# Kernel tuning notes

Measured on AMD Instinct MI355X. Metric: run time of the kernel, lower is better.

Reference implementation:

```python
import jax, jax.numpy as jnp
import numpy as np

# Config (Mamba2-2.7B-like)
HID = 2048          # hidden_size
EXPAND = 2
INTER = EXPAND * HID   # 4096
NH = 64             # num_heads
HD = 64             # head_dim (NH*HD == INTER)
NG = 8              # n_groups
SS = 128            # state_size
CK = 4              # conv_kernel
CH = 256            # chunk_size
EPS = 1e-6
CONV_DIM = INTER + 2 * NG * SS          # 6144
PROJ = INTER + CONV_DIM + NH            # 10304
B_SZ, SEQ = 2, 2048


def segment_sum(x):
    # x: [..., T] -> [..., T, T]; stable cumulative-sum based segment sums
    T = x.shape[-1]
    x = jnp.repeat(x[..., None], T, axis=-1)
    x = jnp.where(jnp.tril(jnp.ones((T, T), dtype=bool), k=-1), x, 0.0)
    s = jnp.cumsum(x, axis=-2)
    return jnp.where(jnp.tril(jnp.ones((T, T), dtype=bool), k=0), s, -jnp.inf)


def setup_inputs() -> dict:
    key = jax.random.key(0)
    ks = jax.random.split(key, 6)
    sc = 0.02
    return {
        "input_states": jax.random.normal(ks[0], (B_SZ, SEQ, HID), dtype=jnp.float32),
        "in_proj_w": jax.random.normal(ks[1], (HID, PROJ), dtype=jnp.float32) * sc,
        "conv_w": jax.random.normal(ks[2], (CK, 1, CONV_DIM), dtype=jnp.float32) * sc,  # WIO, depthwise
        "conv_b": jnp.zeros((CONV_DIM,), dtype=jnp.float32),
        "dt_bias": jnp.ones((NH,), dtype=jnp.float32),
        "A_log": jnp.log(jnp.arange(1, NH + 1, dtype=jnp.float32)),
        "D": jnp.ones((NH,), dtype=jnp.float32),
        "norm_w": jnp.ones((INTER,), dtype=jnp.float32),
        "out_proj_w": jax.random.normal(ks[3], (INTER, HID), dtype=jnp.float32) * sc,
    }


def reference(input_states, in_proj_w, conv_w, conv_b, dt_bias, A_log, D, norm_w, out_proj_w):
    b, s, _ = input_states.shape
    proj = input_states @ in_proj_w                                   # [b,s,PROJ]
    gate, hBC, dt = jnp.split(proj, [INTER, INTER + CONV_DIM], axis=-1)

    # depthwise causal-ish conv (flax nn.Conv with padding='SAME', groups=CONV_DIM)
    hBC = jax.lax.conv_general_dilated(
        hBC, conv_w, window_strides=(1,), padding="SAME",
        dimension_numbers=("NWC", "WIO", "NWC"), feature_group_count=CONV_DIM,
    ) + conv_b
    hBC = jax.nn.silu(hBC)[:, :s]
    hs, Bmat, Cmat = jnp.split(hBC, [INTER, INTER + NG * SS], axis=-1)

    A = -jnp.exp(A_log.astype(jnp.float32))                           # [h]
    dt = jax.nn.softplus(dt + dt_bias)                                # [b,s,h]
    dt = jnp.maximum(dt, 0.0)                                         # time_step_limit (0, inf)

    hs = hs.reshape(b, s, NH, HD).astype(jnp.float32)                 # [b,s,h,p]
    Bmat = Bmat.reshape(b, s, NG, SS).astype(jnp.float32)
    Cmat = Cmat.reshape(b, s, NG, SS).astype(jnp.float32)
    Bmat = jnp.repeat(Bmat, NH // NG, axis=2)                         # [b,s,h,n]
    Cmat = jnp.repeat(Cmat, NH // NG, axis=2)

    pad = (CH - s % CH) % CH

    def to_chunks(t):
        t = jnp.pad(t, [(0, 0), (0, pad)] + [(0, 0)] * (t.ndim - 2))
        return t.reshape(b, -1, CH, *t.shape[2:])

    D_res = D[None, None, :, None] * jnp.pad(hs, [(0, 0), (0, pad), (0, 0), (0, 0)])

    hs_dt = hs * dt[..., None]                                        # discretize x
    A_bt = A[None, None, :] * dt                                      # [b,s,h]

    hs_c = to_chunks(hs_dt)                                           # [b,c,l,h,p]
    A_c = to_chunks(A_bt)                                             # [b,c,l,h]
    B_c = to_chunks(Bmat)                                             # [b,c,l,h,n]
    C_c = to_chunks(Cmat)

    A_p = jnp.transpose(A_c, (0, 3, 1, 2))                            # [b,h,c,l]
    A_cum = jnp.cumsum(A_p, axis=-1)

    # 1. intra-chunk (diagonal blocks)
    L = jnp.exp(segment_sum(A_p))                                     # [b,h,c,l,l]
    M = jnp.einsum("bclhn,bcshn->bclsh", C_c, B_c) * jnp.transpose(L, (0, 2, 3, 4, 1))
    Y_diag = jnp.einsum("bclsh,bcshp->bclhp", M, hs_c)

    # 2. intra-chunk states
    decay_states = jnp.exp(A_cum[..., -1:] - A_cum)                   # [b,h,c,l]
    B_decay = B_c * jnp.transpose(decay_states, (0, 2, 3, 1))[..., None]
    states = jnp.einsum("bclhn,bclhp->bchpn", B_decay, hs_c)          # [b,c,h,p,n]

    # 3. inter-chunk recurrence
    states = jnp.concatenate([jnp.zeros_like(states[:, :1]), states], axis=1)  # [b,c+1,h,p,n]
    A_last = jnp.pad(A_cum[..., -1], [(0, 0), (0, 0), (1, 0)])        # [b,h,c+1]
    decay_chunk = jnp.exp(segment_sum(A_last))                        # [b,h,c+1,c+1]
    new_states = jnp.einsum("bhij,bjhpn->bihpn", decay_chunk, states)
    states_out = new_states[:, :-1]                                   # [b,c,h,p,n]

    # 4. state -> output
    state_decay_out = jnp.exp(A_cum)                                  # [b,h,c,l]
    Y_off = jnp.einsum("bclhn,bchpn->bclhp", C_c, states_out) \
        * jnp.transpose(state_decay_out, (0, 2, 3, 1))[..., None]

    y = (Y_diag + Y_off).reshape(b, -1, NH, HD) + D_res
    y = y[:, :s].reshape(b, s, INTER)

    # gated RMSNorm
    yf = y.astype(jnp.float32) * jax.nn.silu(gate.astype(jnp.float32))
    var = jnp.mean(jnp.square(yf), axis=-1, keepdims=True)
    yn = norm_w * (yf * jax.lax.rsqrt(var + EPS))

    return (yn.astype(input_states.dtype)) @ out_proj_w
```

## Files before the change

kernel.cpp:

```cpp
#include <hip/hip_runtime.h>
#include <hip/hip_bf16.h>


#define S_LEN 2048
#define HIDDEN 2048
#define INTER 4096
#define NH 64
#define HD 64
#define NG 8
#define SSZ 128
#define CONV_DIM 6144
#define PROJ_DIM 10304
#define PROJ_PAD 10496
#define NC 8
#define CHK 256
#define ROWS 4096
#define DT_OFF 10240
#define B_OFF 4096
#define C_OFF 5120

typedef __hip_bfloat16 bf16;
typedef __attribute__((ext_vector_type(8))) short bf16x8;
typedef __attribute__((ext_vector_type(4))) float f32x4;
#define MFMA16(a, b, c) __builtin_amdgcn_mfma_f32_16x16x32_bf16(a, b, c, 0, 0, 0)

union U16x8 { uint4 u; bf16x8 v; };

__device__ __forceinline__ float siluf(float x) { return x / (1.f + __expf(-x)); }
__device__ __forceinline__ float ldf(const float* p) { return *p; }
__device__ __forceinline__ float ldf(const bf16* p) { return __bfloat162float(*p); }
__device__ __forceinline__ unsigned short f2bu(float x) {
  bf16 h = __float2bfloat16(x);
  return __builtin_bit_cast(unsigned short, h);
}
__device__ __forceinline__ float bu2f(unsigned short u) {
  return __uint_as_float(((unsigned)u) << 16);
}
__device__ __forceinline__ unsigned pack2(float lo, float hi) {
  return ((unsigned)f2bu(hi) << 16) | f2bu(lo);
}
__device__ __forceinline__ void gload16(const void* g, void* l) {
  __builtin_amdgcn_global_load_lds((const __attribute__((address_space(1))) unsigned*)g,
                                   (__attribute__((address_space(3))) unsigned*)l, 16, 0, 0);
}

__global__ __launch_bounds__(256) void cvt_bf16_k(const float* __restrict__ x,
                                                  unsigned short* __restrict__ o, int n4) {
  int idx = blockIdx.x * 256 + threadIdx.x;
  int stride = gridDim.x * 256;
  for (int i = idx; i < n4; i += stride) {
    float4 v = reinterpret_cast<const float4*>(x)[i];
    uint2 u = make_uint2(pack2(v.x, v.y), pack2(v.z, v.w));
    reinterpret_cast<uint2*>(o)[i] = u;
  }
}

__global__ __launch_bounds__(256) void add_k(const float* __restrict__ p0,
                                             const float* __restrict__ p1,
                                             float* __restrict__ o, int n4) {
  int idx = blockIdx.x * 256 + threadIdx.x;
  int stride = gridDim.x * 256;
  for (int i = idx; i < n4; i += stride) {
    float4 a = reinterpret_cast<const float4*>(p0)[i];
    float4 b = reinterpret_cast<const float4*>(p1)[i];
    reinterpret_cast<float4*>(o)[i] =
        make_float4(a.x + b.x, a.y + b.y, a.z + b.z, a.w + b.w);
  }
}

__global__ __launch_bounds__(256) void wT_k(const float* __restrict__ W,
                                            unsigned short* __restrict__ Wt,
                                            int K, int N) {
  __shared__ unsigned short t[64][72];
  int n0 = blockIdx.x * 64, k0 = blockIdx.y * 64;
  int tid = threadIdx.x;
  const int fr = tid >> 4;
  const int fc = tid & 15;
#pragma unroll
  for (int i = 0; i < 4; ++i) {
    int kr = fr + i * 16;
    int nc = fc * 4;
    int ng = n0 + nc;
    float4 v = (ng < N) ? *reinterpret_cast<const float4*>(&W[(size_t)(k0 + kr) * N + ng])
                        : make_float4(0.f, 0.f, 0.f, 0.f);
    t[kr][nc] = f2bu(v.x); t[kr][nc + 1] = f2bu(v.y);
    t[kr][nc + 2] = f2bu(v.z); t[kr][nc + 3] = f2bu(v.w);
  }
  __syncthreads();
#pragma unroll
  for (int i = 0; i < 2; ++i) {
    int item = tid + i * 256;
    int nr = item >> 3;
    int kc8 = (item & 7) * 8;
    unsigned short vals[8];
#pragma unroll
    for (int ei = 0; ei < 8; ++ei) {
      int e = ei ^ (tid & 7);
      vals[e] = t[kc8 + e][nr];
    }
    *reinterpret_cast<uint4*>(&Wt[(size_t)(n0 + nr) * K + k0 + kc8]) =
        *reinterpret_cast<const uint4*>(vals);
  }
}

__device__ __forceinline__ int mod9(int x) { return x >= 9 ? x - 9 : x; }

__device__ __forceinline__ void stage_half(const unsigned short* __restrict__ A,
                                           const unsigned short* __restrict__ Bt,
                                           unsigned short* lds9, int hj, int slot,
                                           int m0, int n0, int K, int kbase, int hmax,
                                           int tid, int wid) {
  if (hj >= hmax) return;
  const int t = hj >> 2, i = hj & 3;
  const unsigned short* src = (i < 2) ? A : Bt;
  const int br = ((i < 2) ? m0 : n0) + (i & 1) * 128;
  const int g = (tid & 7) ^ ((tid >> 3) & 7);
#pragma unroll
  for (int r = 0; r < 2; ++r) {
    int row = r * 64 + (tid >> 3);
    gload16(&src[(size_t)(br + row) * K + kbase + t * 64 + g * 8],
            &lds9[slot * 8192 + r * 4096 + wid * 512]);
  }
}

template <typename TC>
__global__ __launch_bounds__(512, 2) void gemm_8ph(const unsigned short* __restrict__ A,
                                                   const unsigned short* __restrict__ Bt,
                                                   TC* __restrict__ C,
                                                   int M, int N, int K, int ksplit) {
  extern __shared__ unsigned short lds9[];
  const int tid = threadIdx.x;
  const int lane = tid & 63, hi = lane >> 4, sl = lane & 15;
  const int wid = tid >> 6;
  const int wm = wid >> 2, wn = wid & 3;
  const int gx = gridDim.x;
  int lin = blockIdx.y * gx + blockIdx.x;
  int cpx = (gx * gridDim.y) >> 3;
  int swz = (lin & 7) * cpx + (lin >> 3);
  const int m0 = (swz / gx) * 256;
  const int n0 = (swz % gx) * 256;
  const int kbase = blockIdx.z * ksplit;
  TC* Cz = C + (size_t)blockIdx.z * M * N;
  const int NT = ksplit >> 6;
  const int HMAX = NT << 2;
  const int rbB = (wn & 1) * 64;

  f32x4 acc[8][4] = {};
  bf16x8 a0[4][2], a1[4][2], bb[4][2];

#pragma unroll
  for (int j = 0; j < 5; ++j)
    stage_half(A, Bt, lds9, j, j, m0, n0, K, kbase, HMAX, tid, wid);

  int j0 = 0;
  for (int t = 0; t < NT; ++t) {
    const int sAw = mod9(j0 + wm);
    const int sBw = mod9(j0 + 2 + (wn >> 1));
    if (4 * t + 4 < HMAX) { asm volatile("s_waitcnt vmcnt(2)" ::: "memory"); }
    else                  { asm volatile("s_waitcnt vmcnt(0)" ::: "memory"); }
    __builtin_amdgcn_sched_barrier(0);
    __builtin_amdgcn_s_barrier();
    __builtin_amdgcn_sched_barrier(0);
#pragma unroll
    for (int mf = 0; mf < 4; ++mf)
#pragma unroll
      for (int kk = 0; kk < 2; ++kk) {
        int ra = mf * 16 + sl;
        a0[mf][kk] = *reinterpret_cast<const bf16x8*>(
            &lds9[sAw * 8192 + ra * 64 + (((kk * 4 + hi) ^ (ra & 7)) * 8)]);
      }
#pragma unroll
    for (int nf = 0; nf < 2; ++nf)
#pragma unroll
      for (int kk = 0; kk < 2; ++kk) {
        int rb = rbB + nf * 16 + sl;
        bb[nf][kk] = *reinterpret_cast<const bf16x8*>(
            &lds9[sBw * 8192 + rb * 64 + (((kk * 4 + hi) ^ (rb & 7)) * 8)]);
      }
    stage_half(A, Bt, lds9, 4 * t + 5, mod9(j0 + 5), m0, n0, K, kbase, HMAX, tid, wid);
    asm volatile("s_waitcnt lgkmcnt(0)" ::: "memory");
    __builtin_amdgcn_sched_barrier(0);
    __builtin_amdgcn_s_setprio(1);
#pragma unroll
    for (int mf = 0; mf < 4; ++mf)
#pragma unroll
      for (int nf = 0; nf < 2; ++nf)
#pragma unroll
        for (int kk = 0; kk < 2; ++kk)
          acc[mf][nf] = MFMA16(a0[mf][kk], bb[nf][kk], acc[mf][nf]);
    __builtin_amdgcn_s_setprio(0);
    __builtin_amdgcn_sched_barrier(0);
#pragma unroll
    for (int nf = 2; nf < 4; ++nf)
#pragma unroll
      for (int kk = 0; kk < 2; ++kk) {
        int rb = rbB + nf * 16 + sl;
        bb[nf][kk] = *reinterpret_cast<const bf16x8*>(
            &lds9[sBw * 8192 + rb * 64 + (((kk * 4 + hi) ^ (rb & 7)) * 8)]);
      }
    stage_half(A, Bt, lds9, 4 * t + 6, mod9(j0 + 6), m0, n0, K, kbase, HMAX, tid, wid);
    asm volatile("s_waitcnt lgkmcnt(0)" ::: "memory");
    __builtin_amdgcn_sched_barrier(0);
    __builtin_amdgcn_s_setprio(1);
#pragma unroll
    for (int mf = 0; mf < 4; ++mf)
#pragma unroll
      for (int nf = 2; nf < 4; ++nf)
#pragma unroll
        for (int kk = 0; kk < 2; ++kk)
          acc[mf][nf] = MFMA16(a0[mf][kk], bb[nf][kk], acc[mf][nf]);
    __builtin_amdgcn_s_setprio(0);
    __builtin_amdgcn_sched_barrier(0);
#pragma unroll
    for (int mf = 0; mf < 4; ++mf)
#pragma unroll
      for (int kk = 0; kk < 2; ++kk) {
        int ra = (mf + 4) * 16 + sl;
        a1[mf][kk] = *reinterpret_cast<const bf16x8*>(
            &lds9[sAw * 8192 + ra * 64 + (((kk * 4 + hi) ^ (ra & 7)) * 8)]);
      }
    stage_half(A, Bt, lds9, 4 * t + 7, mod9(j0 + 7), m0, n0, K, kbase, HMAX, tid, wid);
    asm volatile("s_waitcnt lgkmcnt(0)" ::: "memory");
    __builtin_amdgcn_sched_barrier(0);
    __builtin_amdgcn_s_setprio(1);
#pragma unroll
    for (int mf = 0; mf < 4; ++mf)
#pragma unroll
      for (int nf = 0; nf < 2; ++nf)
#pragma unroll
        for (int kk = 0; kk < 2; ++kk)
          acc[mf + 4][nf] = MFMA16(a1[mf][kk], bb[nf][kk], acc[mf + 4][nf]);
    __builtin_amdgcn_s_setprio(0);
    __builtin_amdgcn_sched_barrier(0);
    stage_half(A, Bt, lds9, 4 * t + 8, mod9(j0 + 8), m0, n0, K, kbase, HMAX, tid, wid);
    __builtin_amdgcn_s_setprio(1);
#pragma unroll
    for (int mf = 0; mf < 4; ++mf)
#pragma unroll
      for (int nf = 2; nf < 4; ++nf)
#pragma unroll
        for (int kk = 0; kk < 2; ++kk)
          acc[mf + 4][nf] = MFMA16(a1[mf][kk], bb[nf][kk], acc[mf + 4][nf]);
    __builtin_amdgcn_s_setprio(0);
    __builtin_amdgcn_sched_barrier(0);
    j0 += 4; if (j0 >= 9) j0 -= 9;
  }
#pragma unroll
  for (int mf = 0; mf < 8; ++mf)
#pragma unroll
    for (int nf = 0; nf < 4; ++nf) {
      int col = n0 + wn * 64 + nf * 16 + sl;
      if (col < N) {
#pragma unroll
        for (int r = 0; r < 4; ++r) {
          int row = m0 + wm * 128 + mf * 16 + hi * 4 + r;
          if constexpr (sizeof(TC) == 2)
            Cz[(size_t)row * N + col] = __float2bfloat16(acc[mf][nf][r]);
          else
            Cz[(size_t)row * N + col] = acc[mf][nf][r];
        }
      }
    }
}

__global__ __launch_bounds__(256) void conv_silu_k(const bf16* __restrict__ proj,
                                                   const float* __restrict__ cw,
                                                   const float* __restrict__ cb,
                                                   bf16* __restrict__ convo) {
  int idx = blockIdx.x * 256 + threadIdx.x;
  int ci = idx % (CONV_DIM / 8);
  int row = idx / (CONV_DIM / 8);
  int c8 = ci * 8;
  int t = row & (S_LEN - 1);
  int b = row >> 11;
  float acc[8];
  {
    float4 b0 = *reinterpret_cast<const float4*>(&cb[c8]);
    float4 b1 = *reinterpret_cast<const float4*>(&cb[c8 + 4]);
    acc[0] = b0.x; acc[1] = b0.y; acc[2] = b0.z; acc[3] = b0.w;
    acc[4] = b1.x; acc[5] = b1.y; acc[6] = b1.z; acc[7] = b1.w;
  }
#pragma unroll
  for (int w = 0; w < 4; w++) {
    int tt = t + w - 1;
    if (tt >= 0 && tt < S_LEN) {
      U16x8 u;
      u.u = *reinterpret_cast<const uint4*>(
          &proj[(size_t)(b * S_LEN + tt) * PROJ_DIM + INTER + c8]);
      float4 w0 = *reinterpret_cast<const float4*>(&cw[w * CONV_DIM + c8]);
      float4 w1 = *reinterpret_cast<const float4*>(&cw[w * CONV_DIM + c8 + 4]);
      acc[0] += w0.x * bu2f((unsigned short)u.v[0]);
      acc[1] += w0.y * bu2f((unsigned short)u.v[1]);
      acc[2] += w0.z * bu2f((unsigned short)u.v[2]);
      acc[3] += w0.w * bu2f((unsigned short)u.v[3]);
      acc[4] += w1.x * bu2f((unsigned short)u.v[4]);
      acc[5] += w1.y * bu2f((unsigned short)u.v[5]);
      acc[6] += w1.z * bu2f((unsigned short)u.v[6]);
      acc[7] += w1.w * bu2f((unsigned short)u.v[7]);
    }
  }
  uint4 o;
  o.x = pack2(siluf(acc[0]), siluf(acc[1]));
  o.y = pack2(siluf(acc[2]), siluf(acc[3]));
  o.z = pack2(siluf(acc[4]), siluf(acc[5]));
  o.w = pack2(siluf(acc[6]), siluf(acc[7]));
  *reinterpret_cast<uint4*>(&convo[(size_t)row * CONV_DIM + c8]) = o;
}

__global__ __launch_bounds__(256) void dt_k(const bf16* __restrict__ proj,
                                            const float* __restrict__ dtb,
                                            float* __restrict__ dtp) {
  int idx = blockIdx.x * 256 + threadIdx.x;
  int h = idx & 63;
  int row = idx >> 6;
  float x = ldf(&proj[(size_t)row * PROJ_DIM + DT_OFF + h]) + dtb[h];
  dtp[idx] = (x > 20.f) ? x : log1pf(__expf(x));
}

__global__ __launch_bounds__(256) void acum_k(const float* __restrict__ dtp,
                                              const float* __restrict__ alog,
                                              float* __restrict__ acum) {
  __shared__ float buf[2][CHK];
  int blk = blockIdx.x;
  int c = blk & 7;
  int h = (blk >> 3) & 63;
  int b = blk >> 9;
  int tid = threadIdx.x;
  int row0 = b * S_LEN + c * CHK;
  float a = -__expf(alog[h]);
  buf[0][tid] = a * dtp[(size_t)(row0 + tid) * NH + h];
  __syncthreads();
  int cur = 0;
#pragma unroll
  for (int off = 1; off < 256; off <<= 1) {
    float nv = buf[cur][tid];
    if (tid >= off) nv += buf[cur][tid - off];
    buf[cur ^ 1][tid] = nv;
    cur ^= 1;
    __syncthreads();
  }
  acum[(size_t)blk * CHK + tid] = buf[cur][tid];
}

__global__ __launch_bounds__(256) void chunk_states_mfma(const bf16* __restrict__ convo,
                                                         const float* __restrict__ dtp,
                                                         const float* __restrict__ acum,
                                                         float* __restrict__ cs) {
  __shared__ float sAc[CHK];
  __shared__ float sDtf[CHK];
  __shared__ float sEx[64];
  __shared__ __align__(16) unsigned short sHT[64 * 64];
  __shared__ __align__(16) unsigned short sBd[128 * 64];
  const int tid = threadIdx.x;
  const int lane = tid & 63, hi = lane >> 4, sl = lane & 15;
  const int wid = tid >> 6, wm = wid >> 1, wn = wid & 1;
  const int blk = blockIdx.x;
  const int h = blk & 63, bc = blk >> 6, c = bc & 7, b = bc >> 3, g = h >> 3;
  const int row0 = b * S_LEN + c * CHK;
  sAc[tid] = acum[((size_t)((b * NH + h) * NC + c)) * CHK + tid];
  sDtf[tid] = dtp[(size_t)(row0 + tid) * NH + h];
  f32x4 acc[2][4] = {};
  for (int ts = 0; ts < 4; ++ts) {
    __syncthreads();
    if (tid < 64) sEx[tid] = __expf(sAc[CHK - 1] - sAc[ts * 64 + tid]);
    __syncthreads();
#pragma unroll
    for (int it = 0; it < 2; ++it) {
      int cid = tid + it * 256;
      int t = cid >> 3, p8 = (cid & 7) * 8;
      U16x8 u;
      u.u = *reinterpret_cast<const uint4*>(
          &convo[(size_t)(row0 + ts * 64 + t) * CONV_DIM + h * HD + p8]);
      float dtv = sDtf[ts * 64 + t];
#pragma unroll
      for (int e = 0; e < 8; ++e) {
        int p = p8 + e;
        int G = (p & 7) ^ ((p >> 3) & 7);
        sHT[p * 64 + (((t >> 3) ^ G) * 8) + (t & 7)] =
            f2bu(bu2f((unsigned short)u.v[e]) * dtv);
      }
    }
#pragma unroll
    for (int it = 0; it < 4; ++it) {
      int cid = tid + it * 256;
      int t = cid >> 4, n8 = (cid & 15) * 8;
      U16x8 u;
      u.u = *reinterpret_cast<const uint4*>(
          &convo[(size_t)(row0 + ts * 64 + t) * CONV_DIM + B_OFF + g * SSZ + n8]);
      float ex = sEx[t];
#pragma unroll
      for (int e = 0; e < 8; ++e) {
        int n = n8 + e;
        int G = (n & 7) ^ ((n >> 3) & 7);
        sBd[n * 64 + (((t >> 3) ^ G) * 8) + (t & 7)] =
            f2bu(bu2f((unsigned short)u.v[e]) * ex);
      }
    }
    __syncthreads();
#pragma unroll
    for (int kc = 0; kc < 2; ++kc) {
      bf16x8 a[2], bb[4];
#pragma unroll
      for (int m = 0; m < 2; ++m) {
        int p = wm * 32 + m * 16 + sl;
        int G = (p & 7) ^ ((p >> 3) & 7);
        a[m] = *reinterpret_cast<const bf16x8*>(
            &sHT[p * 64 + (((kc * 4 + hi) ^ G) * 8)]);
      }
#pragma unroll
      for (int j = 0; j < 4; ++j) {
        int n = wn * 64 + j * 16 + sl;
        int G = (n & 7) ^ ((n >> 3) & 7);
        bb[j] = *reinterpret_cast<const bf16x8*>(
            &sBd[n * 64 + (((kc * 4 + hi) ^ G) * 8)]);
      }
#pragma unroll
      for (int m = 0; m < 2; ++m)
#pragma unroll
        for (int j = 0; j < 4; ++j) acc[m][j] = MFMA16(a[m], bb[j], acc[m][j]);
    }
  }
  size_t base = (size_t)blk * HD * SSZ;
#pragma unroll
  for (int m = 0; m < 2; ++m)
#pragma unroll
    for (int j = 0; j < 4; ++j)
#pragma unroll
      for (int r = 0; r < 4; ++r) {
        int p = wm * 32 + m * 16 + hi * 4 + r;
        int n = wn * 64 + j * 16 + sl;
        cs[base + (size_t)p * SSZ + n] = acc[m][j][r];
      }
}

__global__ __launch_bounds__(256) void chunk_rec_k(const float* __restrict__ acum,
                                                   float* __restrict__ cs) {
  int idx = blockIdx.x * 256 + threadIdx.x;
  int n = idx & 127;
  int p = (idx >> 7) & 63;
  int h = (idx >> 13) & 63;
  int b = idx >> 19;
  float run = 0.f;
#pragma unroll
  for (int c = 0; c < NC; c++) {
    size_t off = ((size_t)(((b * NC + c) * NH + h) * HD + p)) * SSZ + n;
    float csv = cs[off];
    float al = acum[((size_t)((b * NH + h) * NC + c)) * CHK + (CHK - 1)];
    cs[off] = run;
    run = run * __expf(al) + csv;
  }
}

__global__ __launch_bounds__(256) void chunk_out_mfma(const bf16* __restrict__ convo,
                                                      const float* __restrict__ dtp,
                                                      const float* __restrict__ acum,
                                                      const float* __restrict__ cs,
                                                      const float* __restrict__ Dp,
                                                      bf16* __restrict__ yb) {
  __shared__ float sAc[CHK];
  __shared__ float sDt[CHK];
  __shared__ __align__(16) unsigned short sB[64 * 128];
  __shared__ __align__(16) unsigned short sH[64 * 64];
  __shared__ __align__(16) unsigned short sW[4 * 64 * 64];
  const int tid = threadIdx.x;
  const int lane = tid & 63, hi = lane >> 4, sl = lane & 15;
  const int wid = tid >> 6;
  const int blk = blockIdx.x;
  const int h = blk & 63;
  const int bc = blk >> 6;
  const int c = bc & 7;
  const int b = bc >> 3;
  const int g = h >> 3;
  const int row0 = b * S_LEN + c * CHK;
  unsigned short* sWp = &sW[wid * 4096];

  sAc[tid] = acum[((size_t)((b * NH + h) * NC + c)) * CHK + tid];
  sDt[tid] = dtp[(size_t)(row0 + tid) * NH + h];

  bf16x8 cf[4][4];
#pragma unroll
  for (int m = 0; m < 4; ++m)
#pragma unroll
    for (int kc = 0; kc < 4; ++kc) {
      int l = wid * 64 + m * 16 + sl;
      U16x8 u;
      u.u = *reinterpret_cast<const uint4*>(
          &convo[(size_t)(row0 + l) * CONV_DIM + C_OFF + g * SSZ + kc * 32 + hi * 8]);
      cf[m][kc] = u.v;
    }

  f32x4 acc[4][4] = {};

  for (int st = 0; st < 4; ++st) {
    __syncthreads();
#pragma unroll
    for (int it = 0; it < 4; ++it) {
      int cid = tid + it * 256;
      int s = cid >> 4, gr = cid & 15;
      const uint4* p = reinterpret_cast<const uint4*>(
          &convo[(size_t)(row0 + st * 64 + s) * CONV_DIM + B_OFF + g * SSZ + gr * 8]);
      *reinterpret_cast<uint4*>(&sB[s * 128 + (gr ^ (s & 7)) * 8]) = *p;
    }
#pragma unroll
    for (int it = 0; it < 16; ++it) {
      int cid = tid + it * 256;
      int s = cid >> 6, pp = cid & 63;
      float v = ldf(&convo[(size_t)(row0 + st * 64 + s) * CONV_DIM + h * HD + pp]) *
                sDt[st * 64 + s];
      sH[pp * 64 + (((s >> 3) ^ (pp & 7)) * 8) + (s & 7)] = f2bu(v);
    }
    __syncthreads();
    if (wid >= st) {
#pragma unroll
      for (int sf = 0; sf < 4; ++sf) {
        f32x4 d[4] = {};
#pragma unroll
        for (int kc = 0; kc < 4; ++kc) {
          int srow = sf * 16 + sl;
          bf16x8 bfv = *reinterpret_cast<const bf16x8*>(
              &sB[srow * 128 + (((kc * 4 + hi) ^ (srow & 7)) * 8)]);
#pragma unroll
          for (int m = 0; m < 4; ++m) d[m] = MFMA16(cf[m][kc], bfv, d[m]);
        }
        int s_loc = sf * 16 + sl;
        int s_glob = st * 64 + s_loc;
        float acS = sAc[s_glob];
        bool diag = (st == wid);
#pragma unroll
        for (int m = 0; m < 4; ++m)
#pragma unroll
          for (int r = 0; r < 4; ++r) {
            int l_loc = m * 16 + hi * 4 + r;
            int l_glob = wid * 64 + l_loc;
            float e = __expf(sAc[l_glob] - acS);
            float v = d[m][r] * e;
            if (diag && s_glob > l_glob) v = 0.f;
            sWp[l_loc * 64 + (((s_loc >> 3) ^ (l_loc & 7)) * 8) + (s_loc & 7)] = f2bu(v);
          }
      }
    }
    __syncthreads();
    if (wid >= st) {
#pragma unroll
      for (int kc = 0; kc < 2; ++kc) {
        bf16x8 a[4], bb[4];
#pragma unroll
        for (int m = 0; m < 4; ++m) {
          int l = m * 16 + sl;
          a[m] = *reinterpret_cast<const bf16x8*>(
              &sWp[l * 64 + (((kc * 4 + hi) ^ (l & 7)) * 8)]);
        }
#pragma unroll
        for (int j = 0; j < 4; ++j) {
          int p = j * 16 + sl;
          bb[j] = *reinterpret_cast<const bf16x8*>(
              &sH[p * 64 + (((kc * 4 + hi) ^ (p & 7)) * 8)]);
        }
#pragma unroll
        for (int m = 0; m < 4; ++m)
#pragma unroll
          for (int j = 0; j < 4; ++j) acc[m][j] = MFMA16(a[m], bb[j], acc[m][j]);
      }
    }
  }

  __syncthreads();
  {
    size_t sinbase = ((size_t)(((b * NC + c) * NH + h) * HD)) * SSZ;
#pragma unroll
    for (int it = 0; it < 8; ++it) {
      int cid = tid + it * 256;
      int p = cid >> 5, q = cid & 31;
      float4 v = *reinterpret_cast<const float4*>(&cs[sinbase + (size_t)p * SSZ + q * 4]);
      uint2 val = make_uint2(pack2(v.x, v.y), pack2(v.z, v.w));
      *reinterpret_cast<uint2*>(&sB[p * 128 + ((q >> 1) ^ (p & 7)) * 8 + (q & 1) * 4]) = val;
    }
  }
  __syncthreads();
#pragma unroll
  for (int m = 0; m < 4; ++m) {
    float e = __expf(sAc[wid * 64 + m * 16 + sl]);
#pragma unroll
    for (int kc = 0; kc < 4; ++kc) {
      bf16x8 fv = cf[m][kc];
#pragma unroll
      for (int ei = 0; ei < 8; ++ei) {
        unsigned short us = (unsigned short)fv[ei];
        fv[ei] = (short)f2bu(bu2f(us) * e);
      }
      cf[m][kc] = fv;
    }
  }
#pragma unroll
  for (int kc = 0; kc < 4; ++kc) {
    bf16x8 bb[4];
#pragma unroll
    for (int j = 0; j < 4; ++j) {
      int p = j * 16 + sl;
      bb[j] = *reinterpret_cast<const bf16x8*>(
          &sB[p * 128 + (((kc * 4 + hi) ^ (p & 7)) * 8)]);
    }
#pragma unroll
    for (int m = 0; m < 4; ++m)
#pragma unroll
      for (int j = 0; j < 4; ++j) acc[m][j] = MFMA16(cf[m][kc], bb[j], acc[m][j]);
  }

  float Dh = Dp[h];
#pragma unroll
  for (int m = 0; m < 4; ++m)
#pragma unroll
    for (int j = 0; j < 4; ++j)
#pragma unroll
      for (int r = 0; r < 4; ++r) {
        int l_glob = wid * 64 + m * 16 + hi * 4 + r;
        size_t row = (size_t)(row0 + l_glob);
        int pg = j * 16 + sl;
        float hraw = ldf(&convo[row * CONV_DIM + h * HD + pg]);
        yb[row * INTER + h * HD + pg] = __float2bfloat16(acc[m][j][r] + Dh * hraw);
      }
}

__global__ __launch_bounds__(256) void norm_k(const bf16* __restrict__ proj,
                                              const float* __restrict__ nw,
                                              bf16* __restrict__ yb) {
  int row = blockIdx.x;
  int tid = threadIdx.x;
  float vals[16];
  float ss = 0.f;
#pragma unroll
  for (int half = 0; half < 2; half++) {
    int colb = tid * 8 + half * 2048;
    U16x8 gy, gg;
    gy.u = *reinterpret_cast<const uint4*>(&yb[(size_t)row * INTER + colb]);
    gg.u = *reinterpret_cast<const uint4*>(&proj[(size_t)row * PROJ_DIM + colb]);
#pragma unroll
    for (int e = 0; e < 8; e++) {
      float yf = bu2f((unsigned short)gy.v[e]) * siluf(bu2f((unsigned short)gg.v[e]));
      vals[half * 8 + e] = yf;
      ss += yf * yf;
    }
  }
#pragma unroll
  for (int off = 32; off > 0; off >>= 1) ss += __shfl_down(ss, off);
  __shared__ float red[4];
  if ((tid & 63) == 0) red[tid >> 6] = ss;
  __syncthreads();
  float tot = red[0] + red[1] + red[2] + red[3];
  float scale = rsqrtf(tot * (1.f / INTER) + 1e-6f);
#pragma unroll
  for (int half = 0; half < 2; half++) {
    int colb = tid * 8 + half * 2048;
    float4 w0 = *reinterpret_cast<const float4*>(&nw[colb]);
    float4 w1 = *reinterpret_cast<const float4*>(&nw[colb + 4]);
    float s0 = vals[half * 8 + 0] * scale * w0.x, s1 = vals[half * 8 + 1] * scale * w0.y;
    float s2 = vals[half * 8 + 2] * scale * w0.z, s3 = vals[half * 8 + 3] * scale * w0.w;
    float s4 = vals[half * 8 + 4] * scale * w1.x, s5 = vals[half * 8 + 5] * scale * w1.y;
    float s6 = vals[half * 8 + 6] * scale * w1.z, s7 = vals[half * 8 + 7] * scale * w1.w;
    uint4 o = make_uint4(pack2(s0, s1), pack2(s2, s3), pack2(s4, s5), pack2(s6, s7));
    *reinterpret_cast<uint4*>(&yb[(size_t)row * INTER + colb]) = o;
  }
}

extern "C" void kernel_launch(void* const* d_in, const int* in_sizes, int n_in,
                              void* d_out, int out_size, void* d_ws, size_t ws_size,
                              hipStream_t stream) {
  const float* x     = (const float*)d_in[0];
  const float* wproj = (const float*)d_in[1];
  const float* cw    = (const float*)d_in[2];
  const float* cb    = (const float*)d_in[3];
  const float* dtb   = (const float*)d_in[4];
  const float* alog  = (const float*)d_in[5];
  const float* Dp    = (const float*)d_in[6];
  const float* nw    = (const float*)d_in[7];
  const float* wout  = (const float*)d_in[8];
  float* out = (float*)d_out;
  char* ws = (char*)d_ws;

  bf16*  proj  = (bf16*)(ws);
  bf16*  convo = (bf16*)(ws + 84410368);
  bf16*  yb    = (bf16*)(ws + 134742016);
  float* dtp   = (float*)(ws + 168296448);
  float* acum  = (float*)(ws + 169345024);
  float* cs    = (float*)(ws + 170393600);
  unsigned short* Wt1 = (unsigned short*)(ws + 84410368);
  unsigned short* xb  = (unsigned short*)(ws + 134742016);
  unsigned short* Wt2 = (unsigned short*)(ws + 170393600);
  float* part = (float*)(ws);

  hipFuncSetAttribute(reinterpret_cast<const void*>(&gemm_8ph<bf16>),
                      hipFuncAttributeMaxDynamicSharedMemorySize, 147456);
  hipFuncSetAttribute(reinterpret_cast<const void*>(&gemm_8ph<float>),
                      hipFuncAttributeMaxDynamicSharedMemorySize, 147456);

  cvt_bf16_k<<<dim3(2048), 256, 0, stream>>>(x, xb, ROWS * HIDDEN / 4);
  wT_k<<<dim3(PROJ_PAD / 64, HIDDEN / 64), 256, 0, stream>>>(wproj, Wt1, HIDDEN, PROJ_DIM);
  gemm_8ph<bf16><<<dim3(PROJ_PAD / 256, ROWS / 256, 1), 512, 147456, stream>>>(
      xb, Wt1, proj, ROWS, PROJ_DIM, HIDDEN, HIDDEN);
  conv_silu_k<<<dim3(ROWS * CONV_DIM / 8 / 256), 256, 0, stream>>>(proj, cw, cb, convo);
  dt_k<<<dim3(ROWS * NH / 256), 256, 0, stream>>>(proj, dtb, dtp);
  acum_k<<<dim3(2 * NH * NC), 256, 0, stream>>>(dtp, alog, acum);
  chunk_states_mfma<<<dim3(2 * NC * NH), 256, 0, stream>>>(convo, dtp, acum, cs);
  chunk_rec_k<<<dim3(2 * NH * HD * SSZ / 256), 256, 0, stream>>>(acum, cs);
  chunk_out_mfma<<<dim3(2 * NC * NH), 256, 0, stream>>>(convo, dtp, acum, cs, Dp, yb);
  norm_k<<<dim3(ROWS), 256, 0, stream>>>(proj, nw, yb);
  wT_k<<<dim3(HIDDEN / 64, INTER / 64), 256, 0, stream>>>(wout, Wt2, INTER, HIDDEN);
  gemm_8ph<float><<<dim3(HIDDEN / 256, ROWS / 256, 2), 512, 147456, stream>>>(
      (const unsigned short*)yb, Wt2, part, ROWS, HIDDEN, INTER, INTER / 2);
  add_k<<<dim3(2048), 256, 0, stream>>>(part, part + (size_t)ROWS * HIDDEN, out,
                                        ROWS * HIDDEN / 4);
}
```

Before: 507.2 us.

## Balance causal chunk_out work across waves with paired 32-row strips

```diff
diff --git a/kernel.cpp b/kernel.cpp
--- a/kernel.cpp
+++ b/kernel.cpp
@@ -459,9 +459,9 @@
                                                       bf16* __restrict__ yb) {
   __shared__ float sAc[CHK];
   __shared__ float sDt[CHK];
-  __shared__ __align__(16) unsigned short sB[64 * 128];
-  __shared__ __align__(16) unsigned short sH[64 * 64];
-  __shared__ __align__(16) unsigned short sW[4 * 64 * 64];
+  __shared__ __align__(16) unsigned short sB[32 * 128];
+  __shared__ __align__(16) unsigned short sH[64 * 32];
+  __shared__ __align__(16) unsigned short sW[8 * 32 * 32];
   const int tid = threadIdx.x;
   const int lane = tid & 63, hi = lane >> 4, sl = lane & 15;
   const int wid = tid >> 6;
@@ -472,95 +472,114 @@
   const int b = bc >> 3;
   const int g = h >> 3;
   const int row0 = b * S_LEN + c * CHK;
-  unsigned short* sWp = &sW[wid * 4096];
+  const int strips[2] = {wid, 7 - wid};
 
   sAc[tid] = acum[((size_t)((b * NH + h) * NC + c)) * CHK + tid];
   sDt[tid] = dtp[(size_t)(row0 + tid) * NH + h];
 
-  bf16x8 cf[4][4];
-#pragma unroll
-  for (int m = 0; m < 4; ++m)
-#pragma unroll
-    for (int kc = 0; kc < 4; ++kc) {
-      int l = wid * 64 + m * 16 + sl;
-      U16x8 u;
-      u.u = *reinterpret_cast<const uint4*>(
-          &convo[(size_t)(row0 + l) * CONV_DIM + C_OFF + g * SSZ + kc * 32 + hi * 8]);
-      cf[m][kc] = u.v;
-    }
-
-  f32x4 acc[4][4] = {};
-
-  for (int st = 0; st < 4; ++st) {
+  bf16x8 cf[2][2][4];
+#pragma unroll
+  for (int t2 = 0; t2 < 2; ++t2)
+#pragma unroll
+    for (int lf = 0; lf < 2; ++lf)
+#pragma unroll
+      for (int kc = 0; kc < 4; ++kc) {
+        int l = strips[t2] * 32 + lf * 16 + sl;
+        U16x8 u;
+        u.u = *reinterpret_cast<const uint4*>(
+            &convo[(size_t)(row0 + l) * CONV_DIM + C_OFF + g * SSZ + kc * 32 + hi * 8]);
+        cf[t2][lf][kc] = u.v;
+      }
+
+  f32x4 acc[2][2][4] = {};
+
+  for (int st = 0; st < 8; ++st) {
     __syncthreads();
 #pragma unroll
-    for (int it = 0; it < 4; ++it) {
+    for (int it = 0; it < 2; ++it) {
       int cid = tid + it * 256;
       int s = cid >> 4, gr = cid & 15;
       const uint4* p = reinterpret_cast<const uint4*>(
-          &convo[(size_t)(row0 + st * 64 + s) * CONV_DIM + B_OFF + g * SSZ + gr * 8]);
+          &convo[(size_t)(row0 + st * 32 + s) * CONV_DIM + B_OFF + g * SSZ + gr * 8]);
       *reinterpret_cast<uint4*>(&sB[s * 128 + (gr ^ (s & 7)) * 8]) = *p;
     }
-#pragma unroll
-    for (int it = 0; it < 16; ++it) {
-      int cid = tid + it * 256;
-      int s = cid >> 6, pp = cid & 63;
-      float v = ldf(&convo[(size_t)(row0 + st * 64 + s) * CONV_DIM + h * HD + pp]) *
-                sDt[st * 64 + s];
-      sH[pp * 64 + (((s >> 3) ^ (pp & 7)) * 8) + (s & 7)] = f2bu(v);
+    {
+      int s = tid >> 3, p8 = (tid & 7) * 8;
+      U16x8 u;
+      u.u = *reinterpret_cast<const uint4*>(
+          &convo[(size_t)(row0 + st * 32 + s) * CONV_DIM + h * HD + p8]);
+      float dtv = sDt[st * 32 + s];
+#pragma unroll
+      for (int e = 0; e < 8; ++e) {
+        int p = p8 + e;
+        int sw = ((p & 3) ^ ((p >> 2) & 3)) & 3;
+        sH[p * 32 + (((s >> 3) ^ sw) & 3) * 8 + (s & 7)] =
+            f2bu(bu2f((unsigned short)u.v[e]) * dtv);
+      }
     }
     __syncthreads();
-    if (wid >= st) {
-#pragma unroll
-      for (int sf = 0; sf < 4; ++sf) {
-        f32x4 d[4] = {};
-#pragma unroll
-        for (int kc = 0; kc < 4; ++kc) {
-          int srow = sf * 16 + sl;
-          bf16x8 bfv = *reinterpret_cast<const bf16x8*>(
+#pragma unroll
+    for (int t2 = 0; t2 < 2; ++t2) {
+      int is = strips[t2];
+      if (st > is) continue;
+      f32x4 d[2][2] = {};
+#pragma unroll
+      for (int kc = 0; kc < 4; ++kc) {
+        bf16x8 bf2[2];
+#pragma unroll
+        for (int sf2 = 0; sf2 < 2; ++sf2) {
+          int srow = sf2 * 16 + sl;
+          bf2[sf2] = *reinterpret_cast<const bf16x8*>(
               &sB[srow * 128 + (((kc * 4 + hi) ^ (srow & 7)) * 8)]);
-#pragma unroll
-          for (int m = 0; m < 4; ++m) d[m] = MFMA16(cf[m][kc], bfv, d[m]);
         }
-        int s_loc = sf * 16 + sl;
-        int s_glob = st * 64 + s_loc;
-        float acS = sAc[s_glob];
-        bool diag = (st == wid);
-#pragma unroll
-        for (int m = 0; m < 4; ++m)
+#pragma unroll
+        for (int lf = 0; lf < 2; ++lf)
+#pragma unroll
+          for (int sf2 = 0; sf2 < 2; ++sf2)
+            d[lf][sf2] = MFMA16(cf[t2][lf][kc], bf2[sf2], d[lf][sf2]);
+      }
+      unsigned short* sWp = &sW[(wid * 2 + t2) * 1024];
+      bool diag = (st == is);
+#pragma unroll
+      for (int lf = 0; lf < 2; ++lf)
+#pragma unroll
+        for (int sf2 = 0; sf2 < 2; ++sf2) {
+          int s_loc = sf2 * 16 + sl;
+          int s_glob = st * 32 + s_loc;
+          float acS = sAc[s_glob];
 #pragma unroll
           for (int r = 0; r < 4; ++r) {
-            int l_loc = m * 16 + hi * 4 + r;
-            int l_glob = wid * 64 + l_loc;
+            int l_loc = lf * 16 + hi * 4 + r;
+            int l_glob = is * 32 + l_loc;
             float e = __expf(sAc[l_glob] - acS);
-            float v = d[m][r] * e;
+            float v = d[lf][sf2][r] * e;
             if (diag && s_glob > l_glob) v = 0.f;
-            sWp[l_loc * 64 + (((s_loc >> 3) ^ (l_loc & 7)) * 8) + (s_loc & 7)] = f2bu(v);
+            int sw = ((l_loc & 3) ^ ((l_loc >> 2) & 3)) & 3;
+            sWp[l_loc * 32 + (((s_loc >> 3) ^ sw) & 3) * 8 + (s_loc & 7)] = f2bu(v);
           }
-      }
-    }
-    __syncthreads();
-    if (wid >= st) {
-#pragma unroll
-      for (int kc = 0; kc < 2; ++kc) {
-        bf16x8 a[4], bb[4];
-#pragma unroll
-        for (int m = 0; m < 4; ++m) {
-          int l = m * 16 + sl;
-          a[m] = *reinterpret_cast<const bf16x8*>(
-              &sWp[l * 64 + (((kc * 4 + hi) ^ (l & 7)) * 8)]);
         }
-#pragma unroll
-        for (int j = 0; j < 4; ++j) {
-          int p = j * 16 + sl;
-          bb[j] = *reinterpret_cast<const bf16x8*>(
-              &sH[p * 64 + (((kc * 4 + hi) ^ (p & 7)) * 8)]);
-        }
-#pragma unroll
-        for (int m = 0; m < 4; ++m)
-#pragma unroll
-          for (int j = 0; j < 4; ++j) acc[m][j] = MFMA16(a[m], bb[j], acc[m][j]);
-      }
+      asm volatile("s_waitcnt lgkmcnt(0)" ::: "memory");
+      __builtin_amdgcn_sched_barrier(0);
+      bf16x8 aw[2], bh[4];
+#pragma unroll
+      for (int lf = 0; lf < 2; ++lf) {
+        int l = lf * 16 + sl;
+        int sw = ((l & 3) ^ ((l >> 2) & 3)) & 3;
+        aw[lf] = *reinterpret_cast<const bf16x8*>(
+            &sWp[l * 32 + ((hi ^ sw) & 3) * 8]);
+      }
+#pragma unroll
+      for (int pf = 0; pf < 4; ++pf) {
+        int p = pf * 16 + sl;
+        int sw = ((p & 3) ^ ((p >> 2) & 3)) & 3;
+        bh[pf] = *reinterpret_cast<const bf16x8*>(
+            &sH[p * 32 + ((hi ^ sw) & 3) * 8]);
+      }
+#pragma unroll
+      for (int lf = 0; lf < 2; ++lf)
+#pragma unroll
+        for (int pf = 0; pf < 4; ++pf)
+          acc[t2][lf][pf] = MFMA16(aw[lf], bh[pf], acc[t2][lf][pf]);
     }
   }
 
@@ -573,52 +592,60 @@
       int p = cid >> 5, q = cid & 31;
       float4 v = *reinterpret_cast<const float4*>(&cs[sinbase + (size_t)p * SSZ + q * 4]);
       uint2 val = make_uint2(pack2(v.x, v.y), pack2(v.z, v.w));
-      *reinterpret_cast<uint2*>(&sB[p * 128 + ((q >> 1) ^ (p & 7)) * 8 + (q & 1) * 4]) = val;
+      *reinterpret_cast<uint2*>(&sW[p * 128 + ((q >> 1) ^ (p & 7)) * 8 + (q & 1) * 4]) = val;
     }
   }
   __syncthreads();
 #pragma unroll
-  for (int m = 0; m < 4; ++m) {
-    float e = __expf(sAc[wid * 64 + m * 16 + sl]);
-#pragma unroll
-    for (int kc = 0; kc < 4; ++kc) {
-      bf16x8 fv = cf[m][kc];
-#pragma unroll
-      for (int ei = 0; ei < 8; ++ei) {
-        unsigned short us = (unsigned short)fv[ei];
-        fv[ei] = (short)f2bu(bu2f(us) * e);
-      }
-      cf[m][kc] = fv;
-    }
-  }
+  for (int t2 = 0; t2 < 2; ++t2)
+#pragma unroll
+    for (int lf = 0; lf < 2; ++lf) {
+      float e = __expf(sAc[strips[t2] * 32 + lf * 16 + sl]);
+#pragma unroll
+      for (int kc = 0; kc < 4; ++kc) {
+        bf16x8 fv = cf[t2][lf][kc];
+#pragma unroll
+        for (int ei = 0; ei < 8; ++ei) {
+          unsigned short us = (unsigned short)fv[ei];
+          fv[ei] = (short)f2bu(bu2f(us) * e);
+        }
+        cf[t2][lf][kc] = fv;
+      }
+    }
 #pragma unroll
   for (int kc = 0; kc < 4; ++kc) {
-    bf16x8 bb[4];
-#pragma unroll
-    for (int j = 0; j < 4; ++j) {
-      int p = j * 16 + sl;
-      bb[j] = *reinterpret_cast<const bf16x8*>(
-          &sB[p * 128 + (((kc * 4 + hi) ^ (p & 7)) * 8)]);
-    }
-#pragma unroll
-    for (int m = 0; m < 4; ++m)
-#pragma unroll
-      for (int j = 0; j < 4; ++j) acc[m][j] = MFMA16(cf[m][kc], bb[j], acc[m][j]);
+    bf16x8 bs[4];
+#pragma unroll
+    for (int pf = 0; pf < 4; ++pf) {
+      int p = pf * 16 + sl;
+      bs[pf] = *reinterpret_cast<const bf16x8*>(
+          &sW[p * 128 + (((kc * 4 + hi) ^ (p & 7)) * 8)]);
+    }
+#pragma unroll
+    for (int t2 = 0; t2 < 2; ++t2)
+#pragma unroll
+      for (int lf = 0; lf < 2; ++lf)
+#pragma unroll
+        for (int pf = 0; pf < 4; ++pf)
+          acc[t2][lf][pf] = MFMA16(cf[t2][lf][kc], bs[pf], acc[t2][lf][pf]);
   }
 
   float Dh = Dp[h];
 #pragma unroll
-  for (int m = 0; m < 4; ++m)
-#pragma unroll
-    for (int j = 0; j < 4; ++j)
-#pragma unroll
-      for (int r = 0; r < 4; ++r) {
-        int l_glob = wid * 64 + m * 16 + hi * 4 + r;
-        size_t row = (size_t)(row0 + l_glob);
-        int pg = j * 16 + sl;
-        float hraw = ldf(&convo[row * CONV_DIM + h * HD + pg]);
-        yb[row * INTER + h * HD + pg] = __float2bfloat16(acc[m][j][r] + Dh * hraw);
-      }
+  for (int t2 = 0; t2 < 2; ++t2)
+#pragma unroll
+    for (int lf = 0; lf < 2; ++lf)
+#pragma unroll
+      for (int pf = 0; pf < 4; ++pf)
+#pragma unroll
+        for (int r = 0; r < 4; ++r) {
+          int l_glob = strips[t2] * 32 + lf * 16 + hi * 4 + r;
+          size_t row = (size_t)(row0 + l_glob);
+          int pg = pf * 16 + sl;
+          float hraw = ldf(&convo[row * CONV_DIM + h * HD + pg]);
+          yb[row * INTER + h * HD + pg] =
+              __float2bfloat16(acc[t2][lf][pf][r] + Dh * hraw);
+        }
 }
 
 __global__ __launch_bounds__(256) void norm_k(const bf16* __restrict__ proj,
```

After: 516.4 us. No clear change (+1.8%).
